# Performance work log

Hardware: AMD Instinct MI355X
Metric: run time of the kernel (lower is better)

Reference implementation:

```python
import jax, jax.numpy as jnp
import numpy as np

NUM_USERS = 100000
NUM_ITEMS = 100000
D = 64
L = 3
B = 4096
K = 50


def setup_inputs() -> dict:
    key = jax.random.key(0)
    ks = jax.random.split(key, 8)
    user_ids = jax.random.randint(ks[0], (B,), 0, NUM_USERS)
    item_ids = jax.random.randint(ks[1], (B,), 0, NUM_ITEMS)
    social_neighbors = jax.random.randint(ks[2], (B, K), 0, NUM_USERS)
    attention_mask = jax.random.uniform(ks[3], (B, K), dtype=jnp.float32)
    user_table = jax.random.normal(ks[4], (NUM_USERS, D), dtype=jnp.float32) * 0.1
    item_table = jax.random.normal(ks[5], (NUM_ITEMS, D), dtype=jnp.float32) * 0.1
    # xavier-ish scale for the square Linear layers
    Ws = jax.random.normal(ks[6], (L, D, D), dtype=jnp.float32) * (1.0 / np.sqrt(D))
    bs = jnp.zeros((L, D), dtype=jnp.float32)
    return {
        "user_ids": user_ids,
        "item_ids": item_ids,
        "social_neighbors": social_neighbors,
        "attention_mask": attention_mask,
        "user_table": user_table,
        "item_table": item_table,
        "Ws": Ws,
        "bs": bs,
    }


def reference(user_ids, item_ids, social_neighbors, attention_mask,
              user_table, item_table, Ws, bs):
    user_emb = user_table[user_ids]            # [B, D]
    item_emb = item_table[item_ids]            # [B, D]
    neighbor_emb = user_table[social_neighbors]  # [B, K, D]
    mask = attention_mask[..., None]           # [B, K, 1]
    for l in range(Ws.shape[0]):
        # faithful to original: mask is re-applied to neighbor_emb every layer
        neighbor_emb = neighbor_emb * mask
        neighbor_info = jnp.mean(neighbor_emb, axis=1)  # [B, D]
        # nn.Linear: x @ W.T + b
        user_emb = jax.nn.relu((user_emb + neighbor_info) @ Ws[l].T + bs[l])
    scores = user_emb @ item_emb.T              # [B, B]
    return scores
```

## Files before the change

### kernel.cpp

```cpp
#include <hip/hip_runtime.h>
#include <hip/hip_bf16.h>

#define BATCH 4096
#define DIM 64
#define KN 50
#define NL 3

typedef __attribute__((ext_vector_type(8))) short short8;
typedef __attribute__((ext_vector_type(4))) float f32x4;

__global__ __launch_bounds__(256) void gather_kernel(
    const int* __restrict__ user_ids,
    const int* __restrict__ item_ids,
    const int* __restrict__ nbrs,
    const float* __restrict__ mask,
    const float* __restrict__ user_table,
    const float* __restrict__ item_table,
    float* __restrict__ X0,
    float* __restrict__ NM1,
    float* __restrict__ NM2,
    __hip_bfloat16* __restrict__ Iout)
{
    const int tid = threadIdx.x;
    const int wave = tid >> 6;
    const int lane = tid & 63;
    const int b = __builtin_amdgcn_readfirstlane((blockIdx.x << 2) + wave);

    const int it = item_ids[b];
    Iout[b * DIM + lane] = __float2bfloat16(item_table[it * DIM + lane]);

    const int u = user_ids[b];
    const float x = user_table[u * DIM + lane];

    const int* __restrict__ nrow = nbrs + b * KN;
    const float* __restrict__ mrow = mask + b * KN;

    float acc1 = 0.f, acc2 = 0.f, acc3 = 0.f;
    #pragma unroll
    for (int k = 0; k < KN; ++k) {
        const int nk = nrow[k];
        const float wk = mrow[k];
        const float v = user_table[nk * DIM + lane];
        const float w2 = wk * wk;
        acc1 = fmaf(wk, v, acc1);
        acc2 = fmaf(w2, v, acc2);
        acc3 = fmaf(w2 * wk, v, acc3);
    }
    const float inv = 1.0f / (float)KN;
    X0[b * DIM + lane]  = x + acc1 * inv;
    NM1[b * DIM + lane] = acc2 * inv;
    NM2[b * DIM + lane] = acc3 * inv;
}

__global__ __launch_bounds__(256) void mlp_kernel(
    const float* __restrict__ X0,
    const float* __restrict__ NM1,
    const float* __restrict__ NM2,
    const float* __restrict__ Ws,
    const float* __restrict__ bs,
    __hip_bfloat16* __restrict__ Uout)
{
    __shared__ float Wlds[NL * 64 * 65];
    __shared__ float blds[NL * 64];
    __shared__ float4 xb[4][64];

    const int tid = threadIdx.x;

    for (int idx = tid; idx < NL * 64 * 64; idx += 256) {
        const int l = idx >> 12;
        const int rem = idx & 4095;
        const int j = rem >> 6;
        const int i = rem & 63;
        Wlds[l * (64 * 65) + j * 65 + i] = Ws[idx];
    }
    if (tid < NL * 64) blds[tid] = bs[tid];
    __syncthreads();

    const int wave = tid >> 6;
    const int lane = tid & 63;
    const int r0 = (blockIdx.x << 4) + (wave << 2);

    float x0 = X0[(r0 + 0) * DIM + lane];
    float x1 = X0[(r0 + 1) * DIM + lane];
    float x2 = X0[(r0 + 2) * DIM + lane];
    float x3 = X0[(r0 + 3) * DIM + lane];

    #pragma unroll
    for (int l = 0; l < NL; ++l) {
        xb[wave][lane] = make_float4(x0, x1, x2, x3);
        float y0 = blds[l * 64 + lane], y1 = y0, y2 = y0, y3 = y0;
        const float* wrow = &Wlds[l * (64 * 65) + lane * 65];
        #pragma unroll
        for (int i = 0; i < 64; ++i) {
            const float w = wrow[i];
            const float4 xv = xb[wave][i];
            y0 = fmaf(w, xv.x, y0);
            y1 = fmaf(w, xv.y, y1);
            y2 = fmaf(w, xv.z, y2);
            y3 = fmaf(w, xv.w, y3);
        }
        if (l < NL - 1) {
            const float* NM = (l == 0) ? NM1 : NM2;
            x0 = fmaxf(y0, 0.f) + NM[(r0 + 0) * DIM + lane];
            x1 = fmaxf(y1, 0.f) + NM[(r0 + 1) * DIM + lane];
            x2 = fmaxf(y2, 0.f) + NM[(r0 + 2) * DIM + lane];
            x3 = fmaxf(y3, 0.f) + NM[(r0 + 3) * DIM + lane];
        } else {
            x0 = fmaxf(y0, 0.f); x1 = fmaxf(y1, 0.f);
            x2 = fmaxf(y2, 0.f); x3 = fmaxf(y3, 0.f);
        }
    }
    Uout[(r0 + 0) * DIM + lane] = __float2bfloat16(x0);
    Uout[(r0 + 1) * DIM + lane] = __float2bfloat16(x1);
    Uout[(r0 + 2) * DIM + lane] = __float2bfloat16(x2);
    Uout[(r0 + 3) * DIM + lane] = __float2bfloat16(x3);
}

__global__ __launch_bounds__(256) void scores_kernel(
    const __hip_bfloat16* __restrict__ U,
    const __hip_bfloat16* __restrict__ V,
    float* __restrict__ C)
{
    const int tid = threadIdx.x;
    const int wave = tid >> 6;
    const int lane = tid & 63;
    const int quad = lane >> 4;
    const int l16 = lane & 15;

    const int row0 = (blockIdx.y << 6) + (wave << 4);
    const int colG = blockIdx.x << 8;

    const short* Us = (const short*)U;
    const short* Vs = (const short*)V;

    const short* up = Us + (row0 + l16) * DIM + quad * 8;
    const short8 u0 = *(const short8*)(up);
    const short8 u1 = *(const short8*)(up + 32);

    #pragma unroll 4
    for (int ct = 0; ct < 16; ++ct) {
        const int col0 = colG + (ct << 4);
        const short* vp = Vs + (col0 + l16) * DIM + quad * 8;
        const short8 v0 = *(const short8*)(vp);
        const short8 v1 = *(const short8*)(vp + 32);
        f32x4 acc = {0.f, 0.f, 0.f, 0.f};
        acc = __builtin_amdgcn_mfma_f32_16x16x32_bf16(v0, u0, acc, 0, 0, 0);
        acc = __builtin_amdgcn_mfma_f32_16x16x32_bf16(v1, u1, acc, 0, 0, 0);
        float* cp = C + (size_t)(row0 + l16) * BATCH + col0 + (quad << 2);
        *(float4*)cp = make_float4(acc[0], acc[1], acc[2], acc[3]);
    }
}

extern "C" void kernel_launch(void* const* d_in, const int* in_sizes, int n_in,
                              void* d_out, int out_size, void* d_ws, size_t ws_size,
                              hipStream_t stream)
{
    const int* user_ids   = (const int*)d_in[0];
    const int* item_ids   = (const int*)d_in[1];
    const int* nbrs       = (const int*)d_in[2];
    const float* mask     = (const float*)d_in[3];
    const float* utable   = (const float*)d_in[4];
    const float* itable   = (const float*)d_in[5];
    const float* Ws       = (const float*)d_in[6];
    const float* bs       = (const float*)d_in[7];
    float* out = (float*)d_out;

    float* X0  = (float*)d_ws;
    float* NM1 = X0 + BATCH * DIM;
    float* NM2 = NM1 + BATCH * DIM;
    __hip_bfloat16* Ubf = (__hip_bfloat16*)(NM2 + BATCH * DIM);
    __hip_bfloat16* Ibf = Ubf + BATCH * DIM;

    gather_kernel<<<BATCH / 4, 256, 0, stream>>>(user_ids, item_ids, nbrs, mask,
                                                 utable, itable, X0, NM1, NM2, Ibf);
    mlp_kernel<<<BATCH / 16, 256, 0, stream>>>(X0, NM1, NM2, Ws, bs, Ubf);
    scores_kernel<<<dim3(16, 64), 256, 0, stream>>>(Ubf, Ibf, out);
}
```

Baseline: 138.9 us.

## Fuse neighbor gather and MLP into one kernel with vectorized float4 gathers

Merges the gather and MLP kernels into a single 1024-thread block kernel that handles 16 users. The intermediate X0/NM1/NM2 values stay in shared memory instead of making a round trip through global memory, and one launch is removed. The gather now uses float4 loads, with four neighbor groups per wave combined by a cross-lane shuffle reduction. The weight copy into LDS is vectorized, and the scores kernel switches to nontemporal stores. In exchange, each block reloads the full weight set into LDS, only 4 of the 16 waves do the MLP, and the large block size may limit occupancy.

```diff
diff --git a/kernel.cpp b/kernel.cpp
--- a/kernel.cpp
+++ b/kernel.cpp
@@ -9,111 +9,166 @@
 typedef __attribute__((ext_vector_type(8))) short short8;
 typedef __attribute__((ext_vector_type(4))) float f32x4;
 
-__global__ __launch_bounds__(256) void gather_kernel(
+static __device__ __forceinline__ unsigned short f2bf(float f) {
+    union { __hip_bfloat16 h; unsigned short u; } cv;
+    cv.h = __float2bfloat16(f);
+    return cv.u;
+}
+
+__global__ __launch_bounds__(1024) void fused_kernel(
     const int* __restrict__ user_ids,
     const int* __restrict__ item_ids,
     const int* __restrict__ nbrs,
     const float* __restrict__ mask,
     const float* __restrict__ user_table,
     const float* __restrict__ item_table,
-    float* __restrict__ X0,
-    float* __restrict__ NM1,
-    float* __restrict__ NM2,
-    __hip_bfloat16* __restrict__ Iout)
-{
-    const int tid = threadIdx.x;
-    const int wave = tid >> 6;
-    const int lane = tid & 63;
-    const int b = __builtin_amdgcn_readfirstlane((blockIdx.x << 2) + wave);
-
-    const int it = item_ids[b];
-    Iout[b * DIM + lane] = __float2bfloat16(item_table[it * DIM + lane]);
-
-    const int u = user_ids[b];
-    const float x = user_table[u * DIM + lane];
-
-    const int* __restrict__ nrow = nbrs + b * KN;
-    const float* __restrict__ mrow = mask + b * KN;
-
-    float acc1 = 0.f, acc2 = 0.f, acc3 = 0.f;
-    #pragma unroll
-    for (int k = 0; k < KN; ++k) {
-        const int nk = nrow[k];
-        const float wk = mrow[k];
-        const float v = user_table[nk * DIM + lane];
-        const float w2 = wk * wk;
-        acc1 = fmaf(wk, v, acc1);
-        acc2 = fmaf(w2, v, acc2);
-        acc3 = fmaf(w2 * wk, v, acc3);
-    }
-    const float inv = 1.0f / (float)KN;
-    X0[b * DIM + lane]  = x + acc1 * inv;
-    NM1[b * DIM + lane] = acc2 * inv;
-    NM2[b * DIM + lane] = acc3 * inv;
-}
-
-__global__ __launch_bounds__(256) void mlp_kernel(
-    const float* __restrict__ X0,
-    const float* __restrict__ NM1,
-    const float* __restrict__ NM2,
     const float* __restrict__ Ws,
     const float* __restrict__ bs,
-    __hip_bfloat16* __restrict__ Uout)
+    __hip_bfloat16* __restrict__ Uout,
+    __hip_bfloat16* __restrict__ Iout)
 {
     __shared__ float Wlds[NL * 64 * 65];
     __shared__ float blds[NL * 64];
-    __shared__ float4 xb[4][64];
+    __shared__ float xT2[64][16];
+    __shared__ float nm1T2[64][16];
+    __shared__ float nm2T2[64][16];
 
     const int tid = threadIdx.x;
 
-    for (int idx = tid; idx < NL * 64 * 64; idx += 256) {
+    #pragma unroll
+    for (int p = 0; p < 3; ++p) {
+        const int f4 = tid + p * 1024;
+        const int idx = f4 << 2;
         const int l = idx >> 12;
         const int rem = idx & 4095;
         const int j = rem >> 6;
         const int i = rem & 63;
-        Wlds[l * (64 * 65) + j * 65 + i] = Ws[idx];
+        const float4 wv = *reinterpret_cast<const float4*>(&Ws[idx]);
+        *reinterpret_cast<float4*>(&Wlds[l * (64 * 65) + j * 65 + i]) = wv;
     }
     if (tid < NL * 64) blds[tid] = bs[tid];
-    __syncthreads();
 
     const int wave = tid >> 6;
     const int lane = tid & 63;
-    const int r0 = (blockIdx.x << 4) + (wave << 2);
-
-    float x0 = X0[(r0 + 0) * DIM + lane];
-    float x1 = X0[(r0 + 1) * DIM + lane];
-    float x2 = X0[(r0 + 2) * DIM + lane];
-    float x3 = X0[(r0 + 3) * DIM + lane];
-
+    const int g = lane >> 4;
+    const int m = lane & 15;
+    const int b = __builtin_amdgcn_readfirstlane((blockIdx.x << 4) + wave);
+
+    const int it = item_ids[b];
+    const float4 iv = *reinterpret_cast<const float4*>(&item_table[it * DIM + (m << 2)]);
+
+    const int u = user_ids[b];
+    const float4 x = *reinterpret_cast<const float4*>(&user_table[u * DIM + (m << 2)]);
+
+    const int* __restrict__ nrow = nbrs + b * KN;
+    const float* __restrict__ mrow = mask + b * KN;
+
+    float4 a1 = {0.f, 0.f, 0.f, 0.f};
+    float4 a2 = {0.f, 0.f, 0.f, 0.f};
+    float4 a3 = {0.f, 0.f, 0.f, 0.f};
+
+    #pragma unroll
+    for (int t = 0; t < 12; ++t) {
+        const int k = (t << 2) + g;
+        const int nk = nrow[k];
+        const float wk = mrow[k];
+        const float4 v = *reinterpret_cast<const float4*>(&user_table[nk * DIM + (m << 2)]);
+        const float w2 = wk * wk;
+        const float w3 = w2 * wk;
+        a1.x = fmaf(wk, v.x, a1.x); a1.y = fmaf(wk, v.y, a1.y);
+        a1.z = fmaf(wk, v.z, a1.z); a1.w = fmaf(wk, v.w, a1.w);
+        a2.x = fmaf(w2, v.x, a2.x); a2.y = fmaf(w2, v.y, a2.y);
+        a2.z = fmaf(w2, v.z, a2.z); a2.w = fmaf(w2, v.w, a2.w);
+        a3.x = fmaf(w3, v.x, a3.x); a3.y = fmaf(w3, v.y, a3.y);
+        a3.z = fmaf(w3, v.z, a3.z); a3.w = fmaf(w3, v.w, a3.w);
+    }
+    if (g < 2) {
+        const int k = 48 + g;
+        const int nk = nrow[k];
+        const float wk = mrow[k];
+        const float4 v = *reinterpret_cast<const float4*>(&user_table[nk * DIM + (m << 2)]);
+        const float w2 = wk * wk;
+        const float w3 = w2 * wk;
+        a1.x = fmaf(wk, v.x, a1.x); a1.y = fmaf(wk, v.y, a1.y);
+        a1.z = fmaf(wk, v.z, a1.z); a1.w = fmaf(wk, v.w, a1.w);
+        a2.x = fmaf(w2, v.x, a2.x); a2.y = fmaf(w2, v.y, a2.y);
+        a2.z = fmaf(w2, v.z, a2.z); a2.w = fmaf(w2, v.w, a2.w);
+        a3.x = fmaf(w3, v.x, a3.x); a3.y = fmaf(w3, v.y, a3.y);
+        a3.z = fmaf(w3, v.z, a3.z); a3.w = fmaf(w3, v.w, a3.w);
+    }
+
+    a1.x += __shfl_xor(a1.x, 16); a1.y += __shfl_xor(a1.y, 16);
+    a1.z += __shfl_xor(a1.z, 16); a1.w += __shfl_xor(a1.w, 16);
+    a2.x += __shfl_xor(a2.x, 16); a2.y += __shfl_xor(a2.y, 16);
+    a2.z += __shfl_xor(a2.z, 16); a2.w += __shfl_xor(a2.w, 16);
+    a3.x += __shfl_xor(a3.x, 16); a3.y += __shfl_xor(a3.y, 16);
+    a3.z += __shfl_xor(a3.z, 16); a3.w += __shfl_xor(a3.w, 16);
+    a1.x += __shfl_xor(a1.x, 32); a1.y += __shfl_xor(a1.y, 32);
+    a1.z += __shfl_xor(a1.z, 32); a1.w += __shfl_xor(a1.w, 32);
+    a2.x += __shfl_xor(a2.x, 32); a2.y += __shfl_xor(a2.y, 32);
+    a2.z += __shfl_xor(a2.z, 32); a2.w += __shfl_xor(a2.w, 32);
+    a3.x += __shfl_xor(a3.x, 32); a3.y += __shfl_xor(a3.y, 32);
+    a3.z += __shfl_xor(a3.z, 32); a3.w += __shfl_xor(a3.w, 32);
+
+    if (lane < 16) {
+        const float inv = 1.0f / (float)KN;
+        const int i0 = lane << 2;
+        xT2[i0 + 0][wave] = x.x + a1.x * inv;
+        xT2[i0 + 1][wave] = x.y + a1.y * inv;
+        xT2[i0 + 2][wave] = x.z + a1.z * inv;
+        xT2[i0 + 3][wave] = x.w + a1.w * inv;
+        nm1T2[i0 + 0][wave] = a2.x * inv;
+        nm1T2[i0 + 1][wave] = a2.y * inv;
+        nm1T2[i0 + 2][wave] = a2.z * inv;
+        nm1T2[i0 + 3][wave] = a2.w * inv;
+        nm2T2[i0 + 0][wave] = a3.x * inv;
+        nm2T2[i0 + 1][wave] = a3.y * inv;
+        nm2T2[i0 + 2][wave] = a3.z * inv;
+        nm2T2[i0 + 3][wave] = a3.w * inv;
+        ushort4 ip;
+        ip.x = f2bf(iv.x); ip.y = f2bf(iv.y); ip.z = f2bf(iv.z); ip.w = f2bf(iv.w);
+        *reinterpret_cast<ushort4*>(&Iout[b * DIM + i0]) = ip;
+    }
+
+    __syncthreads();
+
+    if (wave >= 4) return;
+    const int w4 = wave << 2;
+
+    float x0, x1, x2, x3;
     #pragma unroll
     for (int l = 0; l < NL; ++l) {
-        xb[wave][lane] = make_float4(x0, x1, x2, x3);
-        float y0 = blds[l * 64 + lane], y1 = y0, y2 = y0, y3 = y0;
+        if (l > 0)
+            *reinterpret_cast<float4*>(&xT2[lane][w4]) = make_float4(x0, x1, x2, x3);
+        float y0 = blds[(l << 6) + lane], y1 = y0, y2 = y0, y3 = y0;
         const float* wrow = &Wlds[l * (64 * 65) + lane * 65];
         #pragma unroll
         for (int i = 0; i < 64; ++i) {
             const float w = wrow[i];
-            const float4 xv = xb[wave][i];
+            const float4 xv = *reinterpret_cast<const float4*>(&xT2[i][w4]);
             y0 = fmaf(w, xv.x, y0);
             y1 = fmaf(w, xv.y, y1);
             y2 = fmaf(w, xv.z, y2);
             y3 = fmaf(w, xv.w, y3);
         }
-        if (l < NL - 1) {
-            const float* NM = (l == 0) ? NM1 : NM2;
-            x0 = fmaxf(y0, 0.f) + NM[(r0 + 0) * DIM + lane];
-            x1 = fmaxf(y1, 0.f) + NM[(r0 + 1) * DIM + lane];
-            x2 = fmaxf(y2, 0.f) + NM[(r0 + 2) * DIM + lane];
-            x3 = fmaxf(y3, 0.f) + NM[(r0 + 3) * DIM + lane];
+        if (l == 0) {
+            const float4 nv = *reinterpret_cast<const float4*>(&nm1T2[lane][w4]);
+            x0 = fmaxf(y0, 0.f) + nv.x; x1 = fmaxf(y1, 0.f) + nv.y;
+            x2 = fmaxf(y2, 0.f) + nv.z; x3 = fmaxf(y3, 0.f) + nv.w;
+        } else if (l == 1) {
+            const float4 nv = *reinterpret_cast<const float4*>(&nm2T2[lane][w4]);
+            x0 = fmaxf(y0, 0.f) + nv.x; x1 = fmaxf(y1, 0.f) + nv.y;
+            x2 = fmaxf(y2, 0.f) + nv.z; x3 = fmaxf(y3, 0.f) + nv.w;
         } else {
             x0 = fmaxf(y0, 0.f); x1 = fmaxf(y1, 0.f);
             x2 = fmaxf(y2, 0.f); x3 = fmaxf(y3, 0.f);
         }
     }
-    Uout[(r0 + 0) * DIM + lane] = __float2bfloat16(x0);
-    Uout[(r0 + 1) * DIM + lane] = __float2bfloat16(x1);
-    Uout[(r0 + 2) * DIM + lane] = __float2bfloat16(x2);
-    Uout[(r0 + 3) * DIM + lane] = __float2bfloat16(x3);
+    const int rb = (blockIdx.x << 4) + w4;
+    Uout[(rb + 0) * DIM + lane] = __float2bfloat16(x0);
+    Uout[(rb + 1) * DIM + lane] = __float2bfloat16(x1);
+    Uout[(rb + 2) * DIM + lane] = __float2bfloat16(x2);
+    Uout[(rb + 3) * DIM + lane] = __float2bfloat16(x3);
 }
 
 __global__ __launch_bounds__(256) void scores_kernel(
@@ -147,7 +202,7 @@
         acc = __builtin_amdgcn_mfma_f32_16x16x32_bf16(v0, u0, acc, 0, 0, 0);
         acc = __builtin_amdgcn_mfma_f32_16x16x32_bf16(v1, u1, acc, 0, 0, 0);
         float* cp = C + (size_t)(row0 + l16) * BATCH + col0 + (quad << 2);
-        *(float4*)cp = make_float4(acc[0], acc[1], acc[2], acc[3]);
+        __builtin_nontemporal_store(acc, (f32x4*)cp);
     }
 }
 
@@ -165,14 +220,10 @@
     const float* bs       = (const float*)d_in[7];
     float* out = (float*)d_out;
 
-    float* X0  = (float*)d_ws;
-    float* NM1 = X0 + BATCH * DIM;
-    float* NM2 = NM1 + BATCH * DIM;
-    __hip_bfloat16* Ubf = (__hip_bfloat16*)(NM2 + BATCH * DIM);
+    __hip_bfloat16* Ubf = (__hip_bfloat16*)d_ws;
     __hip_bfloat16* Ibf = Ubf + BATCH * DIM;
 
-    gather_kernel<<<BATCH / 4, 256, 0, stream>>>(user_ids, item_ids, nbrs, mask,
-                                                 utable, itable, X0, NM1, NM2, Ibf);
-    mlp_kernel<<<BATCH / 16, 256, 0, stream>>>(X0, NM1, NM2, Ws, bs, Ubf);
+    fused_kernel<<<BATCH / 16, 1024, 0, stream>>>(user_ids, item_ids, nbrs, mask,
+                                                  utable, itable, Ws, bs, Ubf, Ibf);
     scores_kernel<<<dim3(16, 64), 256, 0, stream>>>(Ubf, Ibf, out);
 }
```

Measured after the change: 138.4 us. Within noise of the previous version (-0.4%).
